# Kernel optimization log

Hardware: AMD Instinct MI355X
Metric: run time of the kernel (lower is better)

## Reference

```python
import jax, jax.numpy as jnp
import numpy as np

GROUPS = 32
EPS = 1e-5


def setup_inputs() -> dict:
    key = jax.random.key(0)
    ks = jax.random.split(key, 4)
    B, C, H, W = 4, 256, 64, 64
    x = jax.random.normal(ks[0], (B, C, H, W), dtype=jnp.float32)
    gn_w = jnp.ones((C,), jnp.float32)
    gn_b = jnp.zeros((C,), jnp.float32)
    qkv_w = jax.random.normal(ks[1], (3 * C, C), dtype=jnp.float32) * (C ** -0.5)
    qkv_b = jnp.zeros((3 * C,), jnp.float32)
    proj_w = jax.random.normal(ks[2], (C, C), dtype=jnp.float32) * (C ** -0.5)
    proj_b = jnp.zeros((C,), jnp.float32)
    return {"x": x, "gn_w": gn_w, "gn_b": gn_b, "qkv_w": qkv_w,
            "qkv_b": qkv_b, "proj_w": proj_w, "proj_b": proj_b}


def _group_norm(x, w, b):
    B, C, H, W = x.shape
    xr = x.reshape(B, GROUPS, -1)                      # [B, G, (C/G)*H*W]
    mean = xr.mean(axis=-1, keepdims=True)
    var = xr.var(axis=-1, keepdims=True)               # biased, like torch
    h = ((xr - mean) * jax.lax.rsqrt(var + EPS)).reshape(B, C, H, W)
    return h * w[None, :, None, None] + b[None, :, None, None]


def reference(x, gn_w, gn_b, qkv_w, qkv_b, proj_w, proj_b):
    B, C, H, W = x.shape
    h = _group_norm(x, gn_w, gn_b)
    # 1x1 conv == channel GEMM
    qkv = jnp.einsum('oc,bchw->bohw', qkv_w, h) + qkv_b[None, :, None, None]
    qkv = qkv.reshape(B, 3, C, H * W)
    q, k, v = qkv[:, 0], qkv[:, 1], qkv[:, 2]          # [B, C, N]
    scale = C ** (-0.5)
    attn = jax.nn.softmax(jnp.einsum('bci,bcj->bij', q, k) * scale, axis=-1)
    out = jnp.einsum('bij,bcj->bci', attn, v).reshape(B, C, H, W)
    out = jnp.einsum('oc,bchw->bohw', proj_w, out) + proj_b[None, :, None, None]
    return x + out
```

## Files before the change

kernel.cpp:

```cpp
#include <hip/hip_runtime.h>
#include <hip/hip_bf16.h>
#include <math.h>

typedef __bf16 bf16;
typedef __bf16 bf16x8 __attribute__((ext_vector_type(8)));
typedef __bf16 bf16x4 __attribute__((ext_vector_type(4)));
typedef float f32x4 __attribute__((ext_vector_type(4)));

#define MFMA16(a, b, c) __builtin_amdgcn_mfma_f32_16x16x32_bf16(a, b, c, 0, 0, 0)

#define SCALEK 0.09016844005555896f

typedef const __attribute__((address_space(1))) void* gas_t;
typedef __attribute__((address_space(3))) void* las_t;

__global__ __launch_bounds__(256) void gn_kernel(
    const float* __restrict__ x, const float* __restrict__ gw,
    const float* __restrict__ gb, bf16* __restrict__ h) {
  const int bg = blockIdx.x;
  const int b = bg >> 5, g = bg & 31;
  const size_t base = (size_t)(b * 256 + g * 8) * 4096;
  const float* xp = x + base;
  bf16* hp = h + base;
  const int tid = threadIdx.x;

  float s = 0.f, ss = 0.f;
  for (int i = tid * 4; i < 32768; i += 1024) {
    float4 v = *(const float4*)(xp + i);
    s += v.x + v.y + v.z + v.w;
    ss += v.x * v.x + v.y * v.y + v.z * v.z + v.w * v.w;
  }
#pragma unroll
  for (int off = 32; off; off >>= 1) {
    s += __shfl_down(s, off);
    ss += __shfl_down(ss, off);
  }
  __shared__ float red[8];
  if ((tid & 63) == 0) {
    red[(tid >> 6) * 2] = s;
    red[(tid >> 6) * 2 + 1] = ss;
  }
  __syncthreads();
  s = red[0] + red[2] + red[4] + red[6];
  ss = red[1] + red[3] + red[5] + red[7];
  const float mean = s * (1.f / 32768.f);
  const float var = ss * (1.f / 32768.f) - mean * mean;
  const float rstd = rsqrtf(var + 1e-5f);

  for (int i = tid * 4; i < 32768; i += 1024) {
    float4 v = *(const float4*)(xp + i);
    int c = g * 8 + (i >> 12);
    float a = gw[c] * rstd;
    float b2 = gb[c] - mean * a;
    bf16x4 o;
    o[0] = (bf16)(v.x * a + b2);
    o[1] = (bf16)(v.y * a + b2);
    o[2] = (bf16)(v.z * a + b2);
    o[3] = (bf16)(v.w * a + b2);
    *(bf16x4*)(hp + i) = o;
  }
}

__global__ __launch_bounds__(256) void qkv_gemm(
    const bf16* __restrict__ h, const float* __restrict__ w,
    const float* __restrict__ bias, bf16* __restrict__ qt,
    bf16* __restrict__ kt, bf16* __restrict__ vcm) {
  const int b = blockIdx.z;
  const int o0 = blockIdx.y * 64;
  const int p0 = blockIdx.x * 64;
  __shared__ bf16 Alds[64][56];
  __shared__ bf16 Blds[64][56];
  const int tid = threadIdx.x;
  const int lane = tid & 63, wid = tid >> 6;
  const int lr = lane & 15, lg = lane >> 4;
  const int wm = wid >> 1, wn = wid & 1;
  const bf16* hb = h + (size_t)b * 256 * 4096;

  f32x4 acc[2][2] = {};

  for (int k0 = 0; k0 < 256; k0 += 32) {
    {
      int row = tid >> 2, c8 = (tid & 3) * 8;
      const float* src = w + (size_t)(o0 + row) * 256 + k0 + c8;
      float4 v0 = *(const float4*)src;
      float4 v1 = *(const float4*)(src + 4);
      bf16x8 bv;
      bv[0] = (bf16)v0.x; bv[1] = (bf16)v0.y; bv[2] = (bf16)v0.z; bv[3] = (bf16)v0.w;
      bv[4] = (bf16)v1.x; bv[5] = (bf16)v1.y; bv[6] = (bf16)v1.z; bv[7] = (bf16)v1.w;
      *(bf16x8*)&Alds[row][c8] = bv;
    }
    {
      int cc = tid >> 3, p8 = (tid & 7) * 8;
      bf16x8 v = *(const bf16x8*)(hb + (size_t)(k0 + cc) * 4096 + p0 + p8);
#pragma unroll
      for (int e = 0; e < 8; ++e) Blds[p8 + e][cc] = v[e];
    }
    __syncthreads();
    bf16x8 af[2], bfr[2];
#pragma unroll
    for (int mi = 0; mi < 2; ++mi)
      af[mi] = *(const bf16x8*)&Alds[wm * 32 + mi * 16 + lr][lg * 8];
#pragma unroll
    for (int ni = 0; ni < 2; ++ni)
      bfr[ni] = *(const bf16x8*)&Blds[wn * 32 + ni * 16 + lr][lg * 8];
#pragma unroll
    for (int mi = 0; mi < 2; ++mi)
#pragma unroll
      for (int ni = 0; ni < 2; ++ni)
        acc[mi][ni] = MFMA16(af[mi], bfr[ni], acc[mi][ni]);
    __syncthreads();
  }

#pragma unroll
  for (int mi = 0; mi < 2; ++mi) {
#pragma unroll
    for (int ni = 0; ni < 2; ++ni) {
#pragma unroll
      for (int r = 0; r < 4; ++r) {
        int o = o0 + wm * 32 + mi * 16 + lg * 4 + r;
        int p = p0 + wn * 32 + ni * 16 + lr;
        float val = acc[mi][ni][r] + bias[o];
        if (o < 256) {
          qt[((size_t)b * 4096 + p) * 256 + o] = (bf16)val;
        } else if (o < 512) {
          kt[((size_t)b * 4096 + p) * 256 + (o - 256)] = (bf16)(val * SCALEK);
        } else {
          vcm[((size_t)b * 256 + (o - 512)) * 4096 + p] = (bf16)val;
        }
      }
    }
  }
}

template <int S>
__global__ __launch_bounds__(256, 2) void flash_attn(
    const bf16* __restrict__ qt, const bf16* __restrict__ kt,
    const bf16* __restrict__ vcm, bf16* __restrict__ Opart,
    float* __restrict__ l_g) {
  constexpr int NCOMBO = 4 * S;
  constexpr int CSH = (S == 4) ? 4 : (S == 2) ? 3 : 2;
  constexpr int NIT = (4096 / S) / 32;
  const int bid = blockIdx.x;
  const int combo = bid & (NCOMBO - 1);
  const int qtile = bid >> CSH;
  const int b = combo & 3;
  const int split = combo >> 2;
  const int i0 = qtile * 64;
  const int jbase = split * (4096 / S);

  __shared__ bf16 Klds[2][32][256];
  __shared__ bf16 Vlds[2][256][32];
  __shared__ bf16 Plds[64][40];
  __shared__ float lsum[64][2];
  const int tid = threadIdx.x;
  const int lane = tid & 63, w = tid >> 6;
  const int rg = w >> 1, cg = w & 1;
  const int lr = lane & 15, lg = lane >> 4;
  const bf16* qb = qt + (size_t)b * 4096 * 256;
  const bf16* kb = kt + (size_t)b * 4096 * 256;
  const bf16* vb = vcm + (size_t)b * 256 * 4096;

  bf16x8 qa[2][8];
#pragma unroll
  for (int rf = 0; rf < 2; ++rf)
#pragma unroll
    for (int ks = 0; ks < 8; ++ks)
      qa[rf][ks] = *(const bf16x8*)(
          qb + (size_t)(i0 + rg * 32 + rf * 16 + lr) * 256 + ks * 32 + lg * 8);

  float llane[2][4] = {};
  f32x4 accO[2][8] = {};
  const int ksw = (lr & 7) << 3;

  const bf16* kp[4];
  const bf16* vp[4];
#pragma unroll
  for (int it = 0; it < 4; ++it) {
    int chunk = tid + 256 * it;
    int krow = chunk >> 5;
    int kcol = ((chunk & 31) * 8) ^ ((krow & 7) << 3);
    kp[it] = kb + (size_t)(jbase + krow) * 256 + kcol;
    int vrow = chunk >> 2;
    int vcol = (chunk & 3) * 8;
    vp[it] = vb + (size_t)vrow * 4096 + jbase + vcol;
  }

#define STAGE(BUF)                                                            \
  {                                                                           \
    _Pragma("unroll") for (int it = 0; it < 4; ++it) {                        \
      int chunk = tid + 256 * it;                                             \
      __builtin_amdgcn_global_load_lds(                                       \
          (gas_t)(const void*)kp[it],                                         \
          (las_t)(void*)(&Klds[BUF][0][0] + chunk * 8), 16, 0, 0);            \
      __builtin_amdgcn_global_load_lds(                                       \
          (gas_t)(const void*)vp[it],                                         \
          (las_t)(void*)(&Vlds[BUF][0][0] + chunk * 8), 16, 0, 0);            \
      kp[it] += 32 * 256;                                                     \
      vp[it] += 32;                                                           \
    }                                                                         \
  }

  STAGE(0);
  asm volatile("s_waitcnt vmcnt(0)" ::: "memory");
  __builtin_amdgcn_s_barrier();

  for (int jt = 0; jt < NIT; ++jt) {
    const int cur = jt & 1;
    if (jt + 1 < NIT) STAGE(cur ^ 1);

    f32x4 accS[2] = {};
    __builtin_amdgcn_s_setprio(1);
#pragma unroll
    for (int ks = 0; ks < 8; ++ks) {
      bf16x8 kf =
          *(const bf16x8*)&Klds[cur][cg * 16 + lr][(ks * 32 + lg * 8) ^ ksw];
      accS[0] = MFMA16(qa[0][ks], kf, accS[0]);
      accS[1] = MFMA16(qa[1][ks], kf, accS[1]);
    }
    __builtin_amdgcn_s_setprio(0);

#pragma unroll
    for (int rf = 0; rf < 2; ++rf)
#pragma unroll
      for (int r = 0; r < 4; ++r) {
        float p = exp2f(accS[rf][r]);
        llane[rf][r] += p;
        Plds[rg * 32 + rf * 16 + lg * 4 + r][cg * 16 + lr] = (bf16)p;
      }
    asm volatile("s_waitcnt lgkmcnt(0)" ::: "memory");
    __builtin_amdgcn_s_barrier();

    bf16x8 pa0 = *(const bf16x8*)&Plds[rg * 32 + lr][lg * 8];
    bf16x8 pa1 = *(const bf16x8*)&Plds[rg * 32 + 16 + lr][lg * 8];
    __builtin_amdgcn_s_setprio(1);
#pragma unroll
    for (int nf = 0; nf < 8; ++nf) {
      bf16x8 vf =
          *(const bf16x8*)&Vlds[cur][cg * 128 + nf * 16 + lr][lg * 8];
      accO[0][nf] = MFMA16(pa0, vf, accO[0][nf]);
      accO[1][nf] = MFMA16(pa1, vf, accO[1][nf]);
    }
    __builtin_amdgcn_s_setprio(0);

    asm volatile("s_waitcnt vmcnt(0)" ::: "memory");
    __builtin_amdgcn_s_barrier();
  }
#undef STAGE

#pragma unroll
  for (int rf = 0; rf < 2; ++rf)
#pragma unroll
    for (int r = 0; r < 4; ++r) {
      float s = llane[rf][r];
      s += __shfl_xor(s, 1);
      s += __shfl_xor(s, 2);
      s += __shfl_xor(s, 4);
      s += __shfl_xor(s, 8);
      llane[rf][r] = s;
    }
  if (lr == 0) {
#pragma unroll
    for (int rf = 0; rf < 2; ++rf)
#pragma unroll
      for (int r = 0; r < 4; ++r)
        lsum[rg * 32 + rf * 16 + lg * 4 + r][cg] = llane[rf][r];
  }
  asm volatile("s_waitcnt lgkmcnt(0)" ::: "memory");
  __builtin_amdgcn_s_barrier();

  bf16* ob = Opart + ((size_t)(split * 4 + b) * 4096 + i0) * 256;
  const int erow = lane >> 2, ecol = (lane & 3) * 8;
#pragma unroll
  for (int rf = 0; rf < 2; ++rf) {
#pragma unroll
    for (int q = 0; q < 4; ++q) {
#pragma unroll
      for (int r = 0; r < 4; ++r) {
        Plds[w * 16 + lg * 4 + r][lr] = (bf16)(accO[rf][q * 2][r]);
        Plds[w * 16 + lg * 4 + r][16 + lr] = (bf16)(accO[rf][q * 2 + 1][r]);
      }
      bf16x8 val = *(const bf16x8*)&Plds[w * 16 + erow][ecol];
      *(bf16x8*)(ob + (size_t)(rg * 32 + rf * 16 + erow) * 256 + cg * 128 +
                 q * 32 + ecol) = val;
    }
  }
  if (lr == 0 && cg == 0) {
#pragma unroll
    for (int rf = 0; rf < 2; ++rf)
#pragma unroll
      for (int r = 0; r < 4; ++r) {
        int row = rg * 32 + rf * 16 + lg * 4 + r;
        l_g[(size_t)(split * 4 + b) * 4096 + i0 + row] =
            lsum[row][0] + lsum[row][1];
      }
  }
}

template <int S>
__global__ __launch_bounds__(256) void merge_kernel(
    const bf16* __restrict__ Opart, const float* __restrict__ l_g,
    bf16* __restrict__ att) {
  int idx = blockIdx.x * 256 + threadIdx.x;
  int row = idx >> 5, c8 = (idx & 31) * 8;
  float L = 0.f;
#pragma unroll
  for (int s = 0; s < S; ++s) L += l_g[s * 16384 + row];
  float acc[8] = {};
#pragma unroll
  for (int s = 0; s < S; ++s) {
    bf16x8 o = *(const bf16x8*)(Opart + ((size_t)s * 16384 + row) * 256 + c8);
#pragma unroll
    for (int e = 0; e < 8; ++e) acc[e] += (float)o[e];
  }
  float inv = 1.f / L;
  bf16x8 res;
#pragma unroll
  for (int e = 0; e < 8; ++e) res[e] = (bf16)(acc[e] * inv);
  *(bf16x8*)(att + (size_t)row * 256 + c8) = res;
}

__global__ __launch_bounds__(256) void proj_gemm(
    const bf16* __restrict__ att, const float* __restrict__ w,
    const float* __restrict__ bias, const float* __restrict__ x,
    float* __restrict__ out) {
  const int b = blockIdx.z;
  const int o0 = blockIdx.y * 64;
  const int p0 = blockIdx.x * 64;
  __shared__ bf16 Alds[64][56];
  __shared__ bf16 Blds[64][56];
  const int tid = threadIdx.x;
  const int lane = tid & 63, wid = tid >> 6;
  const int lr = lane & 15, lg = lane >> 4;
  const int wm = wid >> 1, wn = wid & 1;
  const bf16* ab = att + (size_t)b * 4096 * 256;

  f32x4 acc[2][2] = {};

  for (int k0 = 0; k0 < 256; k0 += 32) {
    {
      int row = tid >> 2, c8 = (tid & 3) * 8;
      const float* src = w + (size_t)(o0 + row) * 256 + k0 + c8;
      float4 v0 = *(const float4*)src;
      float4 v1 = *(const float4*)(src + 4);
      bf16x8 bv;
      bv[0] = (bf16)v0.x; bv[1] = (bf16)v0.y; bv[2] = (bf16)v0.z; bv[3] = (bf16)v0.w;
      bv[4] = (bf16)v1.x; bv[5] = (bf16)v1.y; bv[6] = (bf16)v1.z; bv[7] = (bf16)v1.w;
      *(bf16x8*)&Alds[row][c8] = bv;
    }
    {
      int pr = tid >> 2, c8 = (tid & 3) * 8;
      *(bf16x8*)&Blds[pr][c8] =
          *(const bf16x8*)(ab + (size_t)(p0 + pr) * 256 + k0 + c8);
    }
    __syncthreads();
    bf16x8 af[2], bfr[2];
#pragma unroll
    for (int mi = 0; mi < 2; ++mi)
      af[mi] = *(const bf16x8*)&Alds[wm * 32 + mi * 16 + lr][lg * 8];
#pragma unroll
    for (int ni = 0; ni < 2; ++ni)
      bfr[ni] = *(const bf16x8*)&Blds[wn * 32 + ni * 16 + lr][lg * 8];
#pragma unroll
    for (int mi = 0; mi < 2; ++mi)
#pragma unroll
      for (int ni = 0; ni < 2; ++ni)
        acc[mi][ni] = MFMA16(af[mi], bfr[ni], acc[mi][ni]);
    __syncthreads();
  }

#pragma unroll
  for (int mi = 0; mi < 2; ++mi) {
#pragma unroll
    for (int ni = 0; ni < 2; ++ni) {
#pragma unroll
      for (int r = 0; r < 4; ++r) {
        int o = o0 + wm * 32 + mi * 16 + lg * 4 + r;
        int p = p0 + wn * 32 + ni * 16 + lr;
        size_t idx = ((size_t)b * 256 + o) * 4096 + p;
        out[idx] = acc[mi][ni][r] + bias[o] + x[idx];
      }
    }
  }
}

extern "C" void kernel_launch(void* const* d_in, const int* in_sizes, int n_in,
                              void* d_out, int out_size, void* d_ws,
                              size_t ws_size, hipStream_t stream) {
  (void)in_sizes; (void)n_in; (void)out_size;
  const float* x = (const float*)d_in[0];
  const float* gn_w = (const float*)d_in[1];
  const float* gn_b = (const float*)d_in[2];
  const float* qkv_w = (const float*)d_in[3];
  const float* qkv_b = (const float*)d_in[4];
  const float* proj_w = (const float*)d_in[5];
  const float* proj_b = (const float*)d_in[6];
  float* out = (float*)d_out;

  const size_t MB = 1024ull * 1024ull;
  char* ws = (char*)d_ws;
  bf16* h = (bf16*)(ws);
  bf16* qt = (bf16*)(ws + 8 * MB);
  bf16* kt = (bf16*)(ws + 16 * MB);
  bf16* vcm = (bf16*)(ws + 24 * MB);

  int S;
  if (ws_size >= 32 * MB + 4 * 8 * MB + 4ull * 16384 * sizeof(float)) S = 4;
  else if (ws_size >= 32 * MB + 2 * 8 * MB + 2ull * 16384 * sizeof(float)) S = 2;
  else S = 1;

  bf16* Opart;
  float* l_g;
  bf16* att = h;
  if (S >= 2) {
    Opart = (bf16*)(ws + 32 * MB);
    l_g = (float*)(ws + 32 * MB + (size_t)S * 8 * MB);
  } else {
    Opart = h;
    l_g = (float*)(ws + 32 * MB);
  }

  gn_kernel<<<128, 256, 0, stream>>>(x, gn_w, gn_b, h);
  qkv_gemm<<<dim3(64, 12, 4), 256, 0, stream>>>(h, qkv_w, qkv_b, qt, kt, vcm);
  if (S == 4) {
    flash_attn<4><<<64 * 16, 256, 0, stream>>>(qt, kt, vcm, Opart, l_g);
    merge_kernel<4><<<2048, 256, 0, stream>>>(Opart, l_g, att);
  } else if (S == 2) {
    flash_attn<2><<<64 * 8, 256, 0, stream>>>(qt, kt, vcm, Opart, l_g);
    merge_kernel<2><<<2048, 256, 0, stream>>>(Opart, l_g, att);
  } else {
    flash_attn<1><<<64 * 4, 256, 0, stream>>>(qt, kt, vcm, Opart, l_g);
    merge_kernel<1><<<2048, 256, 0, stream>>>(Opart, l_g, att);
  }
  proj_gemm<<<dim3(64, 4, 4), 256, 0, stream>>>(att, proj_w, proj_b, x, out);
}
```

Before: 186.1 us.

## Rewrite flash attention with 32x32 MFMA, register-resident P, and 128-row query tiles

The attention kernel now uses 32x32x16 bf16 MFMAs, each wave owning 32 query rows, so a block covers 128 query rows and the grid is halved. The S tile is computed transposed (K as the A operand), so the softmax probabilities can be packed with cvt_pk_bf16 and rearranged with permlane32_swap straight into the B operand of the PV MFMA. This removes the LDS round-trip for P and the mid-iteration barrier. The V tile gets an XOR swizzle and row sums are reduced in registers. The cost is higher register pressure from 16 Q fragments plus 8 f32x16 accumulators, and fewer blocks to spread across CUs.

```diff
diff --git a/kernel.cpp b/kernel.cpp
--- a/kernel.cpp
+++ b/kernel.cpp
@@ -6,8 +6,10 @@
 typedef __bf16 bf16x8 __attribute__((ext_vector_type(8)));
 typedef __bf16 bf16x4 __attribute__((ext_vector_type(4)));
 typedef float f32x4 __attribute__((ext_vector_type(4)));
+typedef float f32x16 __attribute__((ext_vector_type(16)));
 
 #define MFMA16(a, b, c) __builtin_amdgcn_mfma_f32_16x16x32_bf16(a, b, c, 0, 0, 0)
+#define MFMA32(a, b, c) __builtin_amdgcn_mfma_f32_32x32x16_bf16(a, b, c, 0, 0, 0)
 
 #define SCALEK 0.09016844005555896f
 
@@ -145,100 +147,110 @@
   const int qtile = bid >> CSH;
   const int b = combo & 3;
   const int split = combo >> 2;
-  const int i0 = qtile * 64;
+  const int i0 = qtile * 128;
   const int jbase = split * (4096 / S);
 
   __shared__ bf16 Klds[2][32][256];
   __shared__ bf16 Vlds[2][256][32];
-  __shared__ bf16 Plds[64][40];
-  __shared__ float lsum[64][2];
   const int tid = threadIdx.x;
   const int lane = tid & 63, w = tid >> 6;
-  const int rg = w >> 1, cg = w & 1;
-  const int lr = lane & 15, lg = lane >> 4;
+  const int ln = lane & 31;
+  const int hv = lane >> 5;
   const bf16* qb = qt + (size_t)b * 4096 * 256;
   const bf16* kb = kt + (size_t)b * 4096 * 256;
   const bf16* vb = vcm + (size_t)b * 256 * 4096;
 
-  bf16x8 qa[2][8];
-#pragma unroll
-  for (int rf = 0; rf < 2; ++rf)
-#pragma unroll
-    for (int ks = 0; ks < 8; ++ks)
-      qa[rf][ks] = *(const bf16x8*)(
-          qb + (size_t)(i0 + rg * 32 + rf * 16 + lr) * 256 + ks * 32 + lg * 8);
-
-  float llane[2][4] = {};
-  f32x4 accO[2][8] = {};
-  const int ksw = (lr & 7) << 3;
-
-  const bf16* kp[4];
-  const bf16* vp[4];
+  const int qrow = i0 + w * 32 + ln;
+  bf16x8 qf[16];
+#pragma unroll
+  for (int ks = 0; ks < 16; ++ks)
+    qf[ks] = *(const bf16x8*)(qb + (size_t)qrow * 256 + ks * 16 + hv * 8);
+
+  int koff[4], voff[4];
 #pragma unroll
   for (int it = 0; it < 4; ++it) {
     int chunk = tid + 256 * it;
     int krow = chunk >> 5;
-    int kcol = ((chunk & 31) * 8) ^ ((krow & 7) << 3);
-    kp[it] = kb + (size_t)(jbase + krow) * 256 + kcol;
+    koff[it] = krow * 256 + ((((chunk & 31) ^ (krow & 7)) * 8));
     int vrow = chunk >> 2;
-    int vcol = (chunk & 3) * 8;
-    vp[it] = vb + (size_t)vrow * 4096 + jbase + vcol;
-  }
-
-#define STAGE(BUF)                                                            \
+    voff[it] = vrow * 4096 + (((chunk & 3) ^ (vrow & 3)) * 8);
+  }
+
+#define STAGE(JT, BUF)                                                        \
   {                                                                           \
+    const int j0s = jbase + (JT) * 32;                                        \
     _Pragma("unroll") for (int it = 0; it < 4; ++it) {                        \
       int chunk = tid + 256 * it;                                             \
       __builtin_amdgcn_global_load_lds(                                       \
-          (gas_t)(const void*)kp[it],                                         \
+          (gas_t)(const void*)(kb + (size_t)j0s * 256 + koff[it]),            \
           (las_t)(void*)(&Klds[BUF][0][0] + chunk * 8), 16, 0, 0);            \
       __builtin_amdgcn_global_load_lds(                                       \
-          (gas_t)(const void*)vp[it],                                         \
+          (gas_t)(const void*)(vb + (size_t)j0s + voff[it]),                  \
           (las_t)(void*)(&Vlds[BUF][0][0] + chunk * 8), 16, 0, 0);            \
-      kp[it] += 32 * 256;                                                     \
-      vp[it] += 32;                                                           \
     }                                                                         \
   }
 
-  STAGE(0);
+  float llane = 0.f;
+  f32x16 accO[8] = {};
+  const int kswz = ln & 7;
+  const int vswz = ln & 3;
+
+  STAGE(0, 0);
   asm volatile("s_waitcnt vmcnt(0)" ::: "memory");
   __builtin_amdgcn_s_barrier();
 
   for (int jt = 0; jt < NIT; ++jt) {
     const int cur = jt & 1;
-    if (jt + 1 < NIT) STAGE(cur ^ 1);
-
-    f32x4 accS[2] = {};
+    if (jt + 1 < NIT) STAGE(jt + 1, cur ^ 1);
+
+    f32x16 a0 = {}, a1 = {};
     __builtin_amdgcn_s_setprio(1);
 #pragma unroll
     for (int ks = 0; ks < 8; ++ks) {
-      bf16x8 kf =
-          *(const bf16x8*)&Klds[cur][cg * 16 + lr][(ks * 32 + lg * 8) ^ ksw];
-      accS[0] = MFMA16(qa[0][ks], kf, accS[0]);
-      accS[1] = MFMA16(qa[1][ks], kf, accS[1]);
+      bf16x8 kf0 =
+          *(const bf16x8*)&Klds[cur][ln][((2 * ks + hv) ^ kswz) * 8];
+      bf16x8 kf1 =
+          *(const bf16x8*)&Klds[cur][ln][((2 * (ks + 8) + hv) ^ kswz) * 8];
+      a0 = MFMA32(kf0, qf[ks], a0);
+      a1 = MFMA32(kf1, qf[ks + 8], a1);
     }
     __builtin_amdgcn_s_setprio(0);
 
-#pragma unroll
-    for (int rf = 0; rf < 2; ++rf)
-#pragma unroll
-      for (int r = 0; r < 4; ++r) {
-        float p = exp2f(accS[rf][r]);
-        llane[rf][r] += p;
-        Plds[rg * 32 + rf * 16 + lg * 4 + r][cg * 16 + lr] = (bf16)p;
+    float pv[16];
+#pragma unroll
+    for (int r = 0; r < 16; ++r) pv[r] = exp2f(a0[r] + a1[r]);
+    llane += (((pv[0] + pv[1]) + (pv[2] + pv[3])) +
+              ((pv[4] + pv[5]) + (pv[6] + pv[7]))) +
+             (((pv[8] + pv[9]) + (pv[10] + pv[11])) +
+              ((pv[12] + pv[13]) + (pv[14] + pv[15])));
+
+    int pk[8];
+#pragma unroll
+    for (int q4 = 0; q4 < 8; ++q4)
+      asm("v_cvt_pk_bf16_f32 %0, %1, %2"
+          : "=v"(pk[q4])
+          : "v"(pv[q4 * 2]), "v"(pv[q4 * 2 + 1]));
+    bf16x8 pfrag[2];
+#pragma unroll
+    for (int s = 0; s < 2; ++s) {
+      int xa = pk[s * 4 + 0], ya = pk[s * 4 + 2];
+      int xb = pk[s * 4 + 1], yb = pk[s * 4 + 3];
+      asm("v_permlane32_swap_b32 %0, %1" : "+v"(xa), "+v"(ya));
+      asm("v_permlane32_swap_b32 %0, %1" : "+v"(xb), "+v"(yb));
+      union { int i[4]; bf16x8 v; } u;
+      u.i[0] = xa; u.i[1] = xb; u.i[2] = ya; u.i[3] = yb;
+      pfrag[s] = u.v;
+    }
+
+    __builtin_amdgcn_s_setprio(1);
+#pragma unroll
+    for (int s = 0; s < 2; ++s) {
+#pragma unroll
+      for (int cb = 0; cb < 8; ++cb) {
+        bf16x8 vf =
+            *(const bf16x8*)&Vlds[cur][cb * 32 + ln][((2 * s + hv) ^ vswz) * 8];
+        accO[cb] = MFMA32(vf, pfrag[s], accO[cb]);
       }
-    asm volatile("s_waitcnt lgkmcnt(0)" ::: "memory");
-    __builtin_amdgcn_s_barrier();
-
-    bf16x8 pa0 = *(const bf16x8*)&Plds[rg * 32 + lr][lg * 8];
-    bf16x8 pa1 = *(const bf16x8*)&Plds[rg * 32 + 16 + lr][lg * 8];
-    __builtin_amdgcn_s_setprio(1);
-#pragma unroll
-    for (int nf = 0; nf < 8; ++nf) {
-      bf16x8 vf =
-          *(const bf16x8*)&Vlds[cur][cg * 128 + nf * 16 + lr][lg * 8];
-      accO[0][nf] = MFMA16(pa0, vf, accO[0][nf]);
-      accO[1][nf] = MFMA16(pa1, vf, accO[1][nf]);
     }
     __builtin_amdgcn_s_setprio(0);
 
@@ -247,52 +259,29 @@
   }
 #undef STAGE
 
-#pragma unroll
-  for (int rf = 0; rf < 2; ++rf)
-#pragma unroll
-    for (int r = 0; r < 4; ++r) {
-      float s = llane[rf][r];
-      s += __shfl_xor(s, 1);
-      s += __shfl_xor(s, 2);
-      s += __shfl_xor(s, 4);
-      s += __shfl_xor(s, 8);
-      llane[rf][r] = s;
-    }
-  if (lr == 0) {
-#pragma unroll
-    for (int rf = 0; rf < 2; ++rf)
-#pragma unroll
-      for (int r = 0; r < 4; ++r)
-        lsum[rg * 32 + rf * 16 + lg * 4 + r][cg] = llane[rf][r];
-  }
-  asm volatile("s_waitcnt lgkmcnt(0)" ::: "memory");
-  __builtin_amdgcn_s_barrier();
-
-  bf16* ob = Opart + ((size_t)(split * 4 + b) * 4096 + i0) * 256;
-  const int erow = lane >> 2, ecol = (lane & 3) * 8;
-#pragma unroll
-  for (int rf = 0; rf < 2; ++rf) {
-#pragma unroll
-    for (int q = 0; q < 4; ++q) {
-#pragma unroll
-      for (int r = 0; r < 4; ++r) {
-        Plds[w * 16 + lg * 4 + r][lr] = (bf16)(accO[rf][q * 2][r]);
-        Plds[w * 16 + lg * 4 + r][16 + lr] = (bf16)(accO[rf][q * 2 + 1][r]);
-      }
-      bf16x8 val = *(const bf16x8*)&Plds[w * 16 + erow][ecol];
-      *(bf16x8*)(ob + (size_t)(rg * 32 + rf * 16 + erow) * 256 + cg * 128 +
-                 q * 32 + ecol) = val;
-    }
-  }
-  if (lr == 0 && cg == 0) {
-#pragma unroll
-    for (int rf = 0; rf < 2; ++rf)
-#pragma unroll
-      for (int r = 0; r < 4; ++r) {
-        int row = rg * 32 + rf * 16 + lg * 4 + r;
-        l_g[(size_t)(split * 4 + b) * 4096 + i0 + row] =
-            lsum[row][0] + lsum[row][1];
-      }
+  bf16* ob = Opart + ((size_t)(split * 4 + b) * 4096 + qrow) * 256;
+#pragma unroll
+  for (int cb = 0; cb < 8; ++cb) {
+#pragma unroll
+    for (int g = 0; g < 4; ++g) {
+      int lo, hi;
+      asm("v_cvt_pk_bf16_f32 %0, %1, %2"
+          : "=v"(lo)
+          : "v"(accO[cb][g * 4 + 0]), "v"(accO[cb][g * 4 + 1]));
+      asm("v_cvt_pk_bf16_f32 %0, %1, %2"
+          : "=v"(hi)
+          : "v"(accO[cb][g * 4 + 2]), "v"(accO[cb][g * 4 + 3]));
+      int2 val; val.x = lo; val.y = hi;
+      *(int2*)(ob + cb * 32 + g * 8 + hv * 4) = val;
+    }
+  }
+  {
+    int xa = __float_as_int(llane);
+    int ya = xa;
+    asm("v_permlane32_swap_b32 %0, %1" : "+v"(xa), "+v"(ya));
+    float ltot = __int_as_float(xa) + __int_as_float(ya);
+    if (hv == 0)
+      l_g[(size_t)(split * 4 + b) * 4096 + qrow] = ltot;
   }
 }
 
@@ -422,13 +411,13 @@
   gn_kernel<<<128, 256, 0, stream>>>(x, gn_w, gn_b, h);
   qkv_gemm<<<dim3(64, 12, 4), 256, 0, stream>>>(h, qkv_w, qkv_b, qt, kt, vcm);
   if (S == 4) {
-    flash_attn<4><<<64 * 16, 256, 0, stream>>>(qt, kt, vcm, Opart, l_g);
+    flash_attn<4><<<32 * 16, 256, 0, stream>>>(qt, kt, vcm, Opart, l_g);
     merge_kernel<4><<<2048, 256, 0, stream>>>(Opart, l_g, att);
   } else if (S == 2) {
-    flash_attn<2><<<64 * 8, 256, 0, stream>>>(qt, kt, vcm, Opart, l_g);
+    flash_attn<2><<<32 * 8, 256, 0, stream>>>(qt, kt, vcm, Opart, l_g);
     merge_kernel<2><<<2048, 256, 0, stream>>>(Opart, l_g, att);
   } else {
-    flash_attn<1><<<64 * 4, 256, 0, stream>>>(qt, kt, vcm, Opart, l_g);
+    flash_attn<1><<<32 * 4, 256, 0, stream>>>(qt, kt, vcm, Opart, l_g);
     merge_kernel<1><<<2048, 256, 0, stream>>>(Opart, l_g, att);
   }
   proj_gemm<<<dim3(64, 4, 4), 256, 0, stream>>>(att, proj_w, proj_b, x, out);
```

Result: no change. 188.8 us (+1.4%).
